# Kernel tuning notes

Measured on AMD Instinct MI355X. Metric: run time of the kernel, lower is better.

## Reference

```python
import jax, jax.numpy as jnp
import numpy as np

N = 131072   # batch of trajectory points
DX = 2       # state dim (module hardcodes Linear(2,300) in vv)
H_TM = 100   # taskmap coupling-layer hidden
H_VV = 300   # vv net hidden
H_VS = 100   # vel-scalar coupling-layer hidden


def setup_inputs() -> dict:
    key = jax.random.key(0)
    ks = iter(jax.random.split(key, 40))
    def W(i, o):
        return jax.random.normal(next(ks), (i, o), jnp.float32) / np.float32(np.sqrt(i))
    def b(o):
        return 0.01 * jax.random.normal(next(ks), (o,), jnp.float32)
    d = {"x": jax.random.normal(next(ks), (N, DX), jnp.float32)}
    # taskmap CouplingLayer nn1 (tanh MLP, residual)
    d.update(tm1_w1=W(DX, H_TM), tm1_b1=b(H_TM), tm1_w2=W(H_TM, H_TM), tm1_b2=b(H_TM), tm1_w3=W(H_TM, DX), tm1_b3=b(DX))
    # taskmap CouplingLayer nn2_1 (elu MLP -> softplus gate)
    d.update(tm2_w1=W(DX, H_TM), tm2_b1=b(H_TM), tm2_w2=W(H_TM, H_TM), tm2_b2=b(H_TM), tm2_w3=W(H_TM, DX), tm2_b3=b(DX))
    # vv net: Linear(2,300) PReLU Linear(300,300) PReLU Linear(300,2)
    d.update(vv_w1=W(DX, H_VV), vv_b1=b(H_VV), vv_a1=jnp.full((1,), 0.25, jnp.float32),
             vv_w2=W(H_VV, H_VV), vv_b2=b(H_VV), vv_a2=jnp.full((1,), 0.25, jnp.float32),
             vv_w3=W(H_VV, DX), vv_b3=b(DX))
    # log_vel_scalar CouplingLayer nn3 (leaky_relu MLP, residual via broadcast)
    d.update(vs_w1=W(DX, H_VS), vs_b1=b(H_VS), vs_w2=W(H_VS, H_VS), vs_b2=b(H_VS), vs_w3=W(H_VS, 1), vs_b3=b(1))
    return d


def reference(x, tm1_w1, tm1_b1, tm1_w2, tm1_b2, tm1_w3, tm1_b3,
              tm2_w1, tm2_b1, tm2_w2, tm2_b2, tm2_w3, tm2_b3,
              vv_w1, vv_b1, vv_a1, vv_w2, vv_b2, vv_a2, vv_w3, vv_b3,
              vs_w1, vs_b1, vs_w2, vs_b2, vs_w3, vs_b3):
    def taskmap(z):  # CouplingLayer forward with is_diffeomorphism=True; z (..., DX)
        h = jnp.tanh(z @ tm1_w1 + tm1_b1)
        h = jnp.tanh(h @ tm1_w2 + tm1_b2)
        y1 = h @ tm1_w3 + tm1_b3 + z
        g = jax.nn.elu(y1 @ tm2_w1 + tm2_b1)
        g = jax.nn.elu(g @ tm2_w2 + tm2_b2)
        s = jax.nn.softplus(g @ tm2_w3 + tm2_b3)
        return s * y1 + y1

    prelu = lambda t, a: jnp.where(t >= 0, t, a * t)
    leaky = lambda t: jnp.where(t >= 0, t, 0.01 * t)

    origin_y = taskmap(jnp.zeros((1, DX), x.dtype))        # taskmap_fcn(origin)
    y = taskmap(x) - origin_y                              # y_hat (N, DX)
    J = jax.vmap(jax.jacfwd(taskmap))(x)                   # J_hat (N, DX, DX)

    # doty_pre = vv(y_hat)
    h = prelu(y @ vv_w1 + vv_b1, vv_a1)
    h = prelu(h @ vv_w2 + vv_b2, vv_a2)
    doty = h @ vv_w3 + vv_b3                               # (N, DX)

    ls_var = jnp.sum(doty * y, axis=-1, keepdims=True)     # (N, 1)
    V_y = jnp.sum(y * y, axis=-1, keepdims=True)           # (N, 1)
    yd = doty - jax.nn.relu(ls_var + 1e-4 * V_y) * y / (V_y + 1e-12)

    J_inv = jnp.linalg.pinv(J)                             # batched pseudo-inverse
    yd_n = yd / jnp.maximum(jnp.linalg.norm(yd, axis=-1, keepdims=True), 1e-12)  # F.normalize
    xd_hat = jnp.einsum('nij,nj->ni', J_inv, yd_n)         # bmm then squeeze

    # vel_scalar = exp(log_vel_scalar(x)) + eps;  log_vel_scalar = nn3(x) + x  (broadcast (N,1)+(N,DX))
    hs = leaky(x @ vs_w1 + vs_b1)
    hs = leaky(hs @ vs_w2 + vs_b2)
    logv = (hs @ vs_w3 + vs_b3) + x                        # (N, DX) via broadcast
    xd = (jnp.exp(logv) + 1e-12) * xd_hat
    return xd
```

## Files before the change

kernel.cpp:

```cpp
#include <hip/hip_runtime.h>
#include <math.h>

#define H1 100
#define H3 300

#define WT_TM1    0
#define WT_TM2    14336
#define WT_VS     28672
#define WT_VV     43008
#define NSHORT    140288
#define F_TM1W1   0
#define F_TM1B1   256
#define F_TM2W1   384
#define F_TM2B1   640
#define F_VSW1    768
#define F_VSB1    1024
#define F_VVW1    1152
#define F_VVB1    1792
#define F_TM1B2   2112
#define F_TM2B2   2240
#define F_VSB2    2368
#define F_VVB2    2496
#define F_TM1W3T  2816
#define F_TM2W3T  3072
#define F_VSW3T   3328
#define F_VVW3T   3456
#define NFLOAT    4096

typedef __attribute__((ext_vector_type(8))) short s8v;
typedef __attribute__((ext_vector_type(4))) float f4v;

__device__ __forceinline__ f4v mfma16(s8v a, s8v b, f4v c) {
    return __builtin_amdgcn_mfma_f32_16x16x32_bf16(a, b, c, 0, 0, 0);
}
__device__ __forceinline__ float rcp_fast(float v) { return __builtin_amdgcn_rcpf(v); }
__device__ __forceinline__ float tanh_fast(float v) {
    float t = __expf(2.f * v);
    return 1.f - 2.f * rcp_fast(t + 1.f);
}
__device__ __forceinline__ float leakyf(float v) { return v >= 0.f ? v : 0.01f * v; }
__device__ __forceinline__ float preluf(float v, float a) { return v >= 0.f ? v : a * v; }
__device__ __forceinline__ short f2bf(float f) {
    union { float f; unsigned u; } v; v.f = f;
    unsigned r = v.u + 0x7fffu + ((v.u >> 16) & 1u);
    return (short)(r >> 16);
}
#define RED4(v) { v += __shfl_xor(v, 16, 64); v += __shfl_xor(v, 32, 64); }

__global__ void ngdv_prep(
    const float* __restrict__ tm1_w1, const float* __restrict__ tm1_b1,
    const float* __restrict__ tm1_w2, const float* __restrict__ tm1_b2,
    const float* __restrict__ tm1_w3, const float* __restrict__ tm1_b3,
    const float* __restrict__ tm2_w1, const float* __restrict__ tm2_b1,
    const float* __restrict__ tm2_w2, const float* __restrict__ tm2_b2,
    const float* __restrict__ tm2_w3, const float* __restrict__ tm2_b3,
    const float* __restrict__ vs_w1,  const float* __restrict__ vs_b1,
    const float* __restrict__ vs_w2,  const float* __restrict__ vs_b2,
    const float* __restrict__ vs_w3,
    const float* __restrict__ vv_w1,  const float* __restrict__ vv_b1,
    const float* __restrict__ vv_w2,  const float* __restrict__ vv_b2,
    const float* __restrict__ vv_w3,
    short* __restrict__ wsb, float* __restrict__ wsf, float* __restrict__ origin_out)
{
    const int tid = threadIdx.x;
    if (blockIdx.x < 564) {
        int idx = blockIdx.x * 256 + tid;
        if (idx < NSHORT) {
            short o;
            if (idx < WT_VV) {
                int rgn = idx / 14336, r = idx % 14336;
                const float* src = (rgn == 0) ? tm1_w2 : (rgn == 1) ? tm2_w2 : vs_w2;
                int nt = r >> 11, ks = (r >> 9) & 3, lane = (r >> 3) & 63, e = r & 7;
                int n = nt*16 + (lane & 15);
                int k = ks*32 + (lane >> 4)*8 + e;
                o = (n < H1 && k < H1) ? f2bf(src[k*H1 + n]) : (short)0;
            } else {
                int r = idx - WT_VV;
                int nt = r / 5120, rem = r % 5120;
                int ks = rem >> 9, lane = (rem >> 3) & 63, e = r & 7;
                int n = nt*16 + (lane & 15);
                int k = ks*32 + (lane >> 4)*8 + e;
                o = (n < H3 && k < H3) ? f2bf(vv_w2[k*H3 + n]) : (short)0;
            }
            wsb[idx] = o;
        } else {
            int f = idx - NSHORT;
            if (f < NFLOAT) {
                float v = 0.f;
                if (f < 256)       { int d = f >> 7, c = f & 127; if (c < H1) v = tm1_w1[d*H1 + c]; }
                else if (f < 384)  { int c = f - 256;  if (c < H1) v = tm1_b1[c]; }
                else if (f < 640)  { int r = f - 384, d = r >> 7, c = r & 127; if (c < H1) v = tm2_w1[d*H1 + c]; }
                else if (f < 768)  { int c = f - 640;  if (c < H1) v = tm2_b1[c]; }
                else if (f < 1024) { int r = f - 768, d = r >> 7, c = r & 127; if (c < H1) v = vs_w1[d*H1 + c]; }
                else if (f < 1152) { int c = f - 1024; if (c < H1) v = vs_b1[c]; }
                else if (f < 1792) { int r = f - 1152, d = r / 320, c = r % 320; if (c < H3) v = vv_w1[d*H3 + c]; }
                else if (f < 2112) { int c = f - 1792; if (c < H3) v = vv_b1[c]; }
                else if (f < 2240) { int c = f - 2112; if (c < H1) v = tm1_b2[c]; }
                else if (f < 2368) { int c = f - 2240; if (c < H1) v = tm2_b2[c]; }
                else if (f < 2496) { int c = f - 2368; if (c < H1) v = vs_b2[c]; }
                else if (f < 2816) { int c = f - 2496; if (c < H3) v = vv_b2[c]; }
                else if (f < 3072) { int r = f - 2816, i = r >> 7, c = r & 127; if (c < H1) v = tm1_w3[c*2 + i]; }
                else if (f < 3328) { int r = f - 3072, i = r >> 7, c = r & 127; if (c < H1) v = tm2_w3[c*2 + i]; }
                else if (f < 3456) { int c = f - 3328; if (c < H1) v = vs_w3[c]; }
                else               { int r = f - 3456, i = r / 320, c = r % 320; if (c < H3) v = vv_w3[c*2 + i]; }
                wsf[f] = v;
            }
        }
        return;
    }
    __shared__ float h1[H1], h2[H1], y1o[2], g1[H1], g2[H1];
    const int r = tid >> 1, hf = tid & 1;
    const int k0 = hf ? 50 : 0, k1 = hf ? 100 : 50;
    if (tid < H1) h1[tid] = tanhf(tm1_b1[tid]);
    __syncthreads();
    {
        float acc = 0.f;
        if (r < H1) for (int k = k0; k < k1; ++k) acc += h1[k] * tm1_w2[k*H1 + r];
        acc += __shfl_xor(acc, 1, 64);
        if (r < H1 && !hf) h2[r] = tanhf(acc + tm1_b2[r]);
    }
    __syncthreads();
    if (tid < 128) {
        int i = tid >> 6, ln = tid & 63;
        float acc = 0.f;
        if (ln < H1) acc += h2[ln] * tm1_w3[ln*2 + i];
        if (ln + 64 < H1) acc += h2[ln+64] * tm1_w3[(ln+64)*2 + i];
        #pragma unroll
        for (int off = 32; off >= 1; off >>= 1) acc += __shfl_xor(acc, off, 64);
        if (ln == 0) y1o[i] = acc + tm1_b3[i];
    }
    __syncthreads();
    if (tid < H1) {
        float pre = tm2_b1[tid] + y1o[0]*tm2_w1[tid] + y1o[1]*tm2_w1[H1 + tid];
        g1[tid] = pre > 0.f ? pre : expm1f(pre);
    }
    __syncthreads();
    {
        float acc = 0.f;
        if (r < H1) for (int k = k0; k < k1; ++k) acc += g1[k] * tm2_w2[k*H1 + r];
        acc += __shfl_xor(acc, 1, 64);
        if (r < H1 && !hf) { float a = acc + tm2_b2[r]; g2[r] = a > 0.f ? a : expm1f(a); }
    }
    __syncthreads();
    if (tid < 128) {
        int i = tid >> 6, ln = tid & 63;
        float acc = 0.f;
        if (ln < H1) acc += g2[ln] * tm2_w3[ln*2 + i];
        if (ln + 64 < H1) acc += g2[ln+64] * tm2_w3[(ln+64)*2 + i];
        #pragma unroll
        for (int off = 32; off >= 1; off >>= 1) acc += __shfl_xor(acc, off, 64);
        if (ln == 0) {
            float a = acc + tm2_b3[i];
            float s = a > 20.f ? a : log1pf(expf(a));
            origin_out[i] = (1.f + s) * y1o[i];
        }
    }
}

__global__ __launch_bounds__(512, 2) void ngdv_main(
    const float* __restrict__ x,
    const float* __restrict__ tm1_b3, const float* __restrict__ tm2_b3,
    const float* __restrict__ vs_b3,  const float* __restrict__ vv_b3,
    const float* __restrict__ vv_a1,  const float* __restrict__ vv_a2,
    const short* __restrict__ wsb,    const float* __restrict__ wsf,
    const float* __restrict__ origin, float* __restrict__ out, int npts)
{
    __shared__ __align__(16) float LW[4096];
    __shared__ __align__(16) short WB[14336];

    const int tid = threadIdx.x;
    const int wv = tid >> 6, lane = tid & 63;
    const int fm = lane & 15, fq = lane >> 4;
    const int p = blockIdx.x*128 + wv*16 + fm;
    float2 xv = {0.f, 0.f};
    if (p < npts) xv = *(const float2*)&x[p*2];
    const float og0 = origin[0], og1 = origin[1];

    for (int i = tid; i < 1024; i += 512) ((f4v*)LW)[i] = ((const f4v*)wsf)[i];
    {
        const s8v* s = (const s8v*)(wsb + WT_TM1);
        s8v* d = (s8v*)WB;
        for (int i = tid; i < 1792; i += 512) d[i] = s[i];
    }
    __syncthreads();
    const float a1v = vv_a1[0], a2v = vv_a2[0];

    s8v afp[4], aft0[4], aft1[4];

    #pragma unroll
    for (int ks = 0; ks < 4; ++ks) {
        int c0 = ks*32 + fq*8;
        #pragma unroll
        for (int hh = 0; hh < 2; ++hh) {
            f4v w0 = *(const f4v*)&LW[F_TM1W1 + c0 + hh*4];
            f4v w1 = *(const f4v*)&LW[F_TM1W1 + 128 + c0 + hh*4];
            f4v bv = *(const f4v*)&LW[F_TM1B1 + c0 + hh*4];
            #pragma unroll
            for (int e = 0; e < 4; ++e) {
                int ee = hh*4 + e;
                float pre = fmaf(xv.y, w1[e], fmaf(xv.x, w0[e], bv[e]));
                float h = tanh_fast(pre), dd = 1.f - h*h;
                afp[ks][ee] = f2bf(h);
                aft0[ks][ee] = f2bf(w0[e]*dd);
                aft1[ks][ee] = f2bf(w1[e]*dd);
            }
        }
    }

    float y1p0 = 0.f, y1p1 = 0.f, dyp00 = 0.f, dyp01 = 0.f, dyp10 = 0.f, dyp11 = 0.f;
    #pragma unroll
    for (int nt = 0; nt < 7; ++nt) {
        s8v b0 = *(const s8v*)&WB[(nt*4+0)*512 + lane*8];
        s8v b1 = *(const s8v*)&WB[(nt*4+1)*512 + lane*8];
        s8v b2 = *(const s8v*)&WB[(nt*4+2)*512 + lane*8];
        s8v b3 = *(const s8v*)&WB[(nt*4+3)*512 + lane*8];
        f4v cp = {0,0,0,0}, ct0 = {0,0,0,0}, ct1 = {0,0,0,0};
        cp  = mfma16(b0, afp[0], cp);   cp  = mfma16(b1, afp[1], cp);
        cp  = mfma16(b2, afp[2], cp);   cp  = mfma16(b3, afp[3], cp);
        ct0 = mfma16(b0, aft0[0], ct0); ct0 = mfma16(b1, aft0[1], ct0);
        ct0 = mfma16(b2, aft0[2], ct0); ct0 = mfma16(b3, aft0[3], ct0);
        ct1 = mfma16(b0, aft1[0], ct1); ct1 = mfma16(b1, aft1[1], ct1);
        ct1 = mfma16(b2, aft1[2], ct1); ct1 = mfma16(b3, aft1[3], ct1);
        int col0 = nt*16 + fq*4;
        f4v bb2 = *(const f4v*)&LW[F_TM1B2 + col0];
        f4v w0v = *(const f4v*)&LW[F_TM1W3T + col0];
        f4v w1v = *(const f4v*)&LW[F_TM1W3T + 128 + col0];
        #pragma unroll
        for (int r = 0; r < 4; ++r) {
            float h = tanh_fast(cp[r] + bb2[r]);
            float dd = 1.f - h*h;
            float t0 = ct0[r]*dd, t1 = ct1[r]*dd;
            y1p0  = fmaf(h,  w0v[r], y1p0);  y1p1  = fmaf(h,  w1v[r], y1p1);
            dyp00 = fmaf(t0, w0v[r], dyp00); dyp01 = fmaf(t0, w1v[r], dyp01);
            dyp10 = fmaf(t1, w0v[r], dyp10); dyp11 = fmaf(t1, w1v[r], dyp11);
        }
    }
    RED4(y1p0); RED4(y1p1); RED4(dyp00); RED4(dyp01); RED4(dyp10); RED4(dyp11);
    const float y10 = y1p0 + tm1_b3[0] + xv.x;
    const float y11 = y1p1 + tm1_b3[1] + xv.y;
    const float dy00 = dyp00 + 1.f, dy01 = dyp01;
    const float dy10 = dyp10, dy11 = dyp11 + 1.f;
    __syncthreads();

    {
        const s8v* s = (const s8v*)(wsb + WT_TM2);
        s8v* d = (s8v*)WB;
        for (int i = tid; i < 1792; i += 512) d[i] = s[i];
    }
    __syncthreads();

    #pragma unroll
    for (int ks = 0; ks < 4; ++ks) {
        int c0 = ks*32 + fq*8;
        #pragma unroll
        for (int hh = 0; hh < 2; ++hh) {
            f4v w0 = *(const f4v*)&LW[F_TM2W1 + c0 + hh*4];
            f4v w1 = *(const f4v*)&LW[F_TM2W1 + 128 + c0 + hh*4];
            f4v bv = *(const f4v*)&LW[F_TM2B1 + c0 + hh*4];
            #pragma unroll
            for (int e = 0; e < 4; ++e) {
                int ee = hh*4 + e;
                float pre = fmaf(y11, w1[e], fmaf(y10, w0[e], bv[e]));
                float g = pre > 0.f ? pre : (__expf(pre) - 1.f);
                float dd = pre > 0.f ? 1.f : (g + 1.f);
                afp[ks][ee] = f2bf(g);
                aft0[ks][ee] = f2bf((dy00*w0[e] + dy01*w1[e]) * dd);
                aft1[ks][ee] = f2bf((dy10*w0[e] + dy11*w1[e]) * dd);
            }
        }
    }

    float spp0 = 0.f, spp1 = 0.f, dsp00 = 0.f, dsp01 = 0.f, dsp10 = 0.f, dsp11 = 0.f;
    #pragma unroll
    for (int nt = 0; nt < 7; ++nt) {
        s8v b0 = *(const s8v*)&WB[(nt*4+0)*512 + lane*8];
        s8v b1 = *(const s8v*)&WB[(nt*4+1)*512 + lane*8];
        s8v b2 = *(const s8v*)&WB[(nt*4+2)*512 + lane*8];
        s8v b3 = *(const s8v*)&WB[(nt*4+3)*512 + lane*8];
        f4v cp = {0,0,0,0}, ct0 = {0,0,0,0}, ct1 = {0,0,0,0};
        cp  = mfma16(b0, afp[0], cp);   cp  = mfma16(b1, afp[1], cp);
        cp  = mfma16(b2, afp[2], cp);   cp  = mfma16(b3, afp[3], cp);
        ct0 = mfma16(b0, aft0[0], ct0); ct0 = mfma16(b1, aft0[1], ct0);
        ct0 = mfma16(b2, aft0[2], ct0); ct0 = mfma16(b3, aft0[3], ct0);
        ct1 = mfma16(b0, aft1[0], ct1); ct1 = mfma16(b1, aft1[1], ct1);
        ct1 = mfma16(b2, aft1[2], ct1); ct1 = mfma16(b3, aft1[3], ct1);
        int col0 = nt*16 + fq*4;
        f4v bb2 = *(const f4v*)&LW[F_TM2B2 + col0];
        f4v w0v = *(const f4v*)&LW[F_TM2W3T + col0];
        f4v w1v = *(const f4v*)&LW[F_TM2W3T + 128 + col0];
        #pragma unroll
        for (int r = 0; r < 4; ++r) {
            float pre = cp[r] + bb2[r];
            float g = pre > 0.f ? pre : (__expf(pre) - 1.f);
            float dd = pre > 0.f ? 1.f : (g + 1.f);
            float t0 = ct0[r]*dd, t1 = ct1[r]*dd;
            spp0  = fmaf(g,  w0v[r], spp0);  spp1  = fmaf(g,  w1v[r], spp1);
            dsp00 = fmaf(t0, w0v[r], dsp00); dsp01 = fmaf(t0, w1v[r], dsp01);
            dsp10 = fmaf(t1, w0v[r], dsp10); dsp11 = fmaf(t1, w1v[r], dsp11);
        }
    }
    RED4(spp0); RED4(spp1); RED4(dsp00); RED4(dsp01); RED4(dsp10); RED4(dsp11);
    float ys0, ys1, Ja, Jb, Jc, Jd;
    {
        float sp0 = spp0 + tm2_b3[0], sp1 = spp1 + tm2_b3[1];
        float s0 = sp0 > 20.f ? sp0 : __logf(1.f + __expf(sp0));
        float s1 = sp1 > 20.f ? sp1 : __logf(1.f + __expf(sp1));
        float sg0 = rcp_fast(1.f + __expf(-sp0));
        float sg1 = rcp_fast(1.f + __expf(-sp1));
        Ja = dsp00*sg0*y10 + (1.f + s0)*dy00;
        Jb = dsp10*sg0*y10 + (1.f + s0)*dy10;
        Jc = dsp01*sg1*y11 + (1.f + s1)*dy01;
        Jd = dsp11*sg1*y11 + (1.f + s1)*dy11;
        ys0 = (1.f + s0)*y10 - og0;
        ys1 = (1.f + s1)*y11 - og1;
    }
    __syncthreads();

    {
        const s8v* s = (const s8v*)(wsb + WT_VS);
        s8v* d = (s8v*)WB;
        for (int i = tid; i < 1792; i += 512) d[i] = s[i];
    }
    __syncthreads();

    #pragma unroll
    for (int ks = 0; ks < 4; ++ks) {
        int c0 = ks*32 + fq*8;
        #pragma unroll
        for (int hh = 0; hh < 2; ++hh) {
            f4v w0 = *(const f4v*)&LW[F_VSW1 + c0 + hh*4];
            f4v w1 = *(const f4v*)&LW[F_VSW1 + 128 + c0 + hh*4];
            f4v bv = *(const f4v*)&LW[F_VSB1 + c0 + hh*4];
            #pragma unroll
            for (int e = 0; e < 4; ++e)
                afp[ks][hh*4+e] = f2bf(leakyf(fmaf(xv.y, w1[e], fmaf(xv.x, w0[e], bv[e]))));
        }
    }

    float lvp = 0.f;
    #pragma unroll
    for (int nt = 0; nt < 7; ++nt) {
        s8v b0 = *(const s8v*)&WB[(nt*4+0)*512 + lane*8];
        s8v b1 = *(const s8v*)&WB[(nt*4+1)*512 + lane*8];
        s8v b2 = *(const s8v*)&WB[(nt*4+2)*512 + lane*8];
        s8v b3 = *(const s8v*)&WB[(nt*4+3)*512 + lane*8];
        f4v cp = {0,0,0,0};
        cp = mfma16(b0, afp[0], cp); cp = mfma16(b1, afp[1], cp);
        cp = mfma16(b2, afp[2], cp); cp = mfma16(b3, afp[3], cp);
        int col0 = nt*16 + fq*4;
        f4v bb2 = *(const f4v*)&LW[F_VSB2 + col0];
        f4v w0v = *(const f4v*)&LW[F_VSW3T + col0];
        #pragma unroll
        for (int r = 0; r < 4; ++r)
            lvp = fmaf(leakyf(cp[r] + bb2[r]), w0v[r], lvp);
    }
    RED4(lvp);
    const float lv = lvp + vs_b3[0];
    __syncthreads();

    {
        const s8v* s = (const s8v*)(wsb + WT_VV);
        s8v* d = (s8v*)WB;
        for (int i = tid; i < 640; i += 512) d[i] = s[i];
    }
    s8v afw[10];
    #pragma unroll
    for (int ks = 0; ks < 10; ++ks) {
        int c0 = ks*32 + fq*8;
        #pragma unroll
        for (int hh = 0; hh < 2; ++hh) {
            f4v w0 = *(const f4v*)&LW[F_VVW1 + c0 + hh*4];
            f4v w1 = *(const f4v*)&LW[F_VVW1 + 320 + c0 + hh*4];
            f4v bv = *(const f4v*)&LW[F_VVB1 + c0 + hh*4];
            #pragma unroll
            for (int e = 0; e < 4; ++e)
                afw[ks][hh*4+e] = f2bf(preluf(fmaf(ys1, w1[e], fmaf(ys0, w0[e], bv[e])), a1v));
        }
    }
    __syncthreads();

    float dtp0 = 0.f, dtp1 = 0.f;
    for (int t = 0; t < 19; ++t) {
        if (t < 18) {
            const s8v* s = (const s8v*)(wsb + WT_VV + (t+1)*5120);
            s8v* d = (s8v*)(WB + ((t+1) & 1)*5120);
            for (int i = tid; i < 640; i += 512) d[i] = s[i];
        }
        const short* VB = WB + (t & 1)*5120;
        f4v cp = {0,0,0,0};
        #pragma unroll
        for (int ks = 0; ks < 10; ++ks) {
            s8v bf = *(const s8v*)&VB[ks*512 + lane*8];
            cp = mfma16(bf, afw[ks], cp);
        }
        int col0 = t*16 + fq*4;
        f4v bb2 = *(const f4v*)&LW[F_VVB2 + col0];
        f4v w0v = *(const f4v*)&LW[F_VVW3T + col0];
        f4v w1v = *(const f4v*)&LW[F_VVW3T + 320 + col0];
        #pragma unroll
        for (int r = 0; r < 4; ++r) {
            float v = preluf(cp[r] + bb2[r], a2v);
            dtp0 = fmaf(v, w0v[r], dtp0);
            dtp1 = fmaf(v, w1v[r], dtp1);
        }
        __syncthreads();
    }
    RED4(dtp0); RED4(dtp1);
    const float dt0 = dtp0 + vv_b3[0];
    const float dt1 = dtp1 + vv_b3[1];

    if (fq == 0 && p < npts) {
        float ls = dt0*ys0 + dt1*ys1;
        float Vq = ys0*ys0 + ys1*ys1;
        float coef = fmaxf(ls + 1e-4f*Vq, 0.f) * rcp_fast(Vq + 1e-12f);
        float yd0 = dt0 - coef*ys0, yd1 = dt1 - coef*ys1;
        float inv_n = rcp_fast(fmaxf(sqrtf(yd0*yd0 + yd1*yd1), 1e-12f));
        float yn0 = yd0*inv_n, yn1 = yd1*inv_n;
        float invdet = rcp_fast(Ja*Jd - Jb*Jc);
        float xh0 = ( Jd*yn0 - Jb*yn1) * invdet;
        float xh1 = (-Jc*yn0 + Ja*yn1) * invdet;
        float2 o;
        o.x = (__expf(lv + xv.x) + 1e-12f) * xh0;
        o.y = (__expf(lv + xv.y) + 1e-12f) * xh1;
        *(float2*)&out[p*2] = o;
    }
}

extern "C" void kernel_launch(void* const* d_in, const int* in_sizes, int n_in,
                              void* d_out, int out_size, void* d_ws, size_t ws_size,
                              hipStream_t stream) {
    const float* x      = (const float*)d_in[0];
    const float* tm1_w1 = (const float*)d_in[1];
    const float* tm1_b1 = (const float*)d_in[2];
    const float* tm1_w2 = (const float*)d_in[3];
    const float* tm1_b2 = (const float*)d_in[4];
    const float* tm1_w3 = (const float*)d_in[5];
    const float* tm1_b3 = (const float*)d_in[6];
    const float* tm2_w1 = (const float*)d_in[7];
    const float* tm2_b1 = (const float*)d_in[8];
    const float* tm2_w2 = (const float*)d_in[9];
    const float* tm2_b2 = (const float*)d_in[10];
    const float* tm2_w3 = (const float*)d_in[11];
    const float* tm2_b3 = (const float*)d_in[12];
    const float* vv_w1  = (const float*)d_in[13];
    const float* vv_b1  = (const float*)d_in[14];
    const float* vv_a1  = (const float*)d_in[15];
    const float* vv_w2  = (const float*)d_in[16];
    const float* vv_b2  = (const float*)d_in[17];
    const float* vv_a2  = (const float*)d_in[18];
    const float* vv_w3  = (const float*)d_in[19];
    const float* vv_b3  = (const float*)d_in[20];
    const float* vs_w1  = (const float*)d_in[21];
    const float* vs_b1  = (const float*)d_in[22];
    const float* vs_w2  = (const float*)d_in[23];
    const float* vs_b2  = (const float*)d_in[24];
    const float* vs_w3  = (const float*)d_in[25];
    const float* vs_b3  = (const float*)d_in[26];

    float* out       = (float*)d_out;
    float* origin_ws = (float*)d_ws;
    short* wsb       = (short*)((char*)d_ws + 64);
    float* wsf       = (float*)((char*)d_ws + 64 + NSHORT*2);
    const int npts = in_sizes[0] / 2;
    const int nblk = (npts + 127) / 128;

    ngdv_prep<<<565, 256, 0, stream>>>(
        tm1_w1, tm1_b1, tm1_w2, tm1_b2, tm1_w3, tm1_b3,
        tm2_w1, tm2_b1, tm2_w2, tm2_b2, tm2_w3, tm2_b3,
        vs_w1, vs_b1, vs_w2, vs_b2, vs_w3,
        vv_w1, vv_b1, vv_w2, vv_b2, vv_w3,
        wsb, wsf, origin_ws);

    ngdv_main<<<nblk, 512, 0, stream>>>(
        x, tm1_b3, tm2_b3, vs_b3, vv_b3, vv_a1, vv_a2,
        wsb, wsf, origin_ws, out, npts);
}
```

Measured before the change: 255.5 us.

## Halve block size to 256 threads and read first-layer weights from global memory

Shrinks the main kernel's block from 512 to 256 threads (64 points per block, launch bounds 256,4), doubling the grid. It also stops staging the first-layer weights and biases in shared memory and reads them straight from the global workspace, which halves the float shared buffer. The aim is to raise occupancy and cut per-block shared memory and barrier cost. In exchange each block now copies the full bf16 weight tiles for half as many points, and the first-layer loads go through the cache hierarchy instead of LDS.

```diff
diff --git a/kernel.cpp b/kernel.cpp
--- a/kernel.cpp
+++ b/kernel.cpp
@@ -26,6 +26,8 @@
 #define F_VSW3T   3328
 #define F_VVW3T   3456
 #define NFLOAT    4096
+#define LWB       2112
+#define LWN       1984
 
 typedef __attribute__((ext_vector_type(8))) short s8v;
 typedef __attribute__((ext_vector_type(4))) float f4v;
@@ -157,7 +159,7 @@
     }
 }
 
-__global__ __launch_bounds__(512, 2) void ngdv_main(
+__global__ __launch_bounds__(256, 4) void ngdv_main(
     const float* __restrict__ x,
     const float* __restrict__ tm1_b3, const float* __restrict__ tm2_b3,
     const float* __restrict__ vs_b3,  const float* __restrict__ vv_b3,
@@ -165,22 +167,22 @@
     const short* __restrict__ wsb,    const float* __restrict__ wsf,
     const float* __restrict__ origin, float* __restrict__ out, int npts)
 {
-    __shared__ __align__(16) float LW[4096];
+    __shared__ __align__(16) float LW[2048];
     __shared__ __align__(16) short WB[14336];
 
     const int tid = threadIdx.x;
     const int wv = tid >> 6, lane = tid & 63;
     const int fm = lane & 15, fq = lane >> 4;
-    const int p = blockIdx.x*128 + wv*16 + fm;
+    const int p = blockIdx.x*64 + wv*16 + fm;
     float2 xv = {0.f, 0.f};
     if (p < npts) xv = *(const float2*)&x[p*2];
     const float og0 = origin[0], og1 = origin[1];
 
-    for (int i = tid; i < 1024; i += 512) ((f4v*)LW)[i] = ((const f4v*)wsf)[i];
+    for (int i = tid; i < 496; i += 256) ((f4v*)LW)[i] = *(const f4v*)&wsf[LWB + i*4];
     {
         const s8v* s = (const s8v*)(wsb + WT_TM1);
         s8v* d = (s8v*)WB;
-        for (int i = tid; i < 1792; i += 512) d[i] = s[i];
+        for (int i = tid; i < 1792; i += 256) d[i] = s[i];
     }
     __syncthreads();
     const float a1v = vv_a1[0], a2v = vv_a2[0];
@@ -192,9 +194,9 @@
         int c0 = ks*32 + fq*8;
         #pragma unroll
         for (int hh = 0; hh < 2; ++hh) {
-            f4v w0 = *(const f4v*)&LW[F_TM1W1 + c0 + hh*4];
-            f4v w1 = *(const f4v*)&LW[F_TM1W1 + 128 + c0 + hh*4];
-            f4v bv = *(const f4v*)&LW[F_TM1B1 + c0 + hh*4];
+            f4v w0 = *(const f4v*)&wsf[F_TM1W1 + c0 + hh*4];
+            f4v w1 = *(const f4v*)&wsf[F_TM1W1 + 128 + c0 + hh*4];
+            f4v bv = *(const f4v*)&wsf[F_TM1B1 + c0 + hh*4];
             #pragma unroll
             for (int e = 0; e < 4; ++e) {
                 int ee = hh*4 + e;
@@ -222,9 +224,9 @@
         ct1 = mfma16(b0, aft1[0], ct1); ct1 = mfma16(b1, aft1[1], ct1);
         ct1 = mfma16(b2, aft1[2], ct1); ct1 = mfma16(b3, aft1[3], ct1);
         int col0 = nt*16 + fq*4;
-        f4v bb2 = *(const f4v*)&LW[F_TM1B2 + col0];
-        f4v w0v = *(const f4v*)&LW[F_TM1W3T + col0];
-        f4v w1v = *(const f4v*)&LW[F_TM1W3T + 128 + col0];
+        f4v bb2 = *(const f4v*)&LW[F_TM1B2 - LWB + col0];
+        f4v w0v = *(const f4v*)&LW[F_TM1W3T - LWB + col0];
+        f4v w1v = *(const f4v*)&LW[F_TM1W3T + 128 - LWB + col0];
         #pragma unroll
         for (int r = 0; r < 4; ++r) {
             float h = tanh_fast(cp[r] + bb2[r]);
@@ -245,7 +247,7 @@
     {
         const s8v* s = (const s8v*)(wsb + WT_TM2);
         s8v* d = (s8v*)WB;
-        for (int i = tid; i < 1792; i += 512) d[i] = s[i];
+        for (int i = tid; i < 1792; i += 256) d[i] = s[i];
     }
     __syncthreads();
 
@@ -254,9 +256,9 @@
         int c0 = ks*32 + fq*8;
         #pragma unroll
         for (int hh = 0; hh < 2; ++hh) {
-            f4v w0 = *(const f4v*)&LW[F_TM2W1 + c0 + hh*4];
-            f4v w1 = *(const f4v*)&LW[F_TM2W1 + 128 + c0 + hh*4];
-            f4v bv = *(const f4v*)&LW[F_TM2B1 + c0 + hh*4];
+            f4v w0 = *(const f4v*)&wsf[F_TM2W1 + c0 + hh*4];
+            f4v w1 = *(const f4v*)&wsf[F_TM2W1 + 128 + c0 + hh*4];
+            f4v bv = *(const f4v*)&wsf[F_TM2B1 + c0 + hh*4];
             #pragma unroll
             for (int e = 0; e < 4; ++e) {
                 int ee = hh*4 + e;
@@ -285,9 +287,9 @@
         ct1 = mfma16(b0, aft1[0], ct1); ct1 = mfma16(b1, aft1[1], ct1);
         ct1 = mfma16(b2, aft1[2], ct1); ct1 = mfma16(b3, aft1[3], ct1);
         int col0 = nt*16 + fq*4;
-        f4v bb2 = *(const f4v*)&LW[F_TM2B2 + col0];
-        f4v w0v = *(const f4v*)&LW[F_TM2W3T + col0];
-        f4v w1v = *(const f4v*)&LW[F_TM2W3T + 128 + col0];
+        f4v bb2 = *(const f4v*)&LW[F_TM2B2 - LWB + col0];
+        f4v w0v = *(const f4v*)&LW[F_TM2W3T - LWB + col0];
+        f4v w1v = *(const f4v*)&LW[F_TM2W3T + 128 - LWB + col0];
         #pragma unroll
         for (int r = 0; r < 4; ++r) {
             float pre = cp[r] + bb2[r];
@@ -319,7 +321,7 @@
     {
         const s8v* s = (const s8v*)(wsb + WT_VS);
         s8v* d = (s8v*)WB;
-        for (int i = tid; i < 1792; i += 512) d[i] = s[i];
+        for (int i = tid; i < 1792; i += 256) d[i] = s[i];
     }
     __syncthreads();
 
@@ -328,9 +330,9 @@
         int c0 = ks*32 + fq*8;
         #pragma unroll
         for (int hh = 0; hh < 2; ++hh) {
-            f4v w0 = *(const f4v*)&LW[F_VSW1 + c0 + hh*4];
-            f4v w1 = *(const f4v*)&LW[F_VSW1 + 128 + c0 + hh*4];
-            f4v bv = *(const f4v*)&LW[F_VSB1 + c0 + hh*4];
+            f4v w0 = *(const f4v*)&wsf[F_VSW1 + c0 + hh*4];
+            f4v w1 = *(const f4v*)&wsf[F_VSW1 + 128 + c0 + hh*4];
+            f4v bv = *(const f4v*)&wsf[F_VSB1 + c0 + hh*4];
             #pragma unroll
             for (int e = 0; e < 4; ++e)
                 afp[ks][hh*4+e] = f2bf(leakyf(fmaf(xv.y, w1[e], fmaf(xv.x, w0[e], bv[e]))));
@@ -348,8 +350,8 @@
         cp = mfma16(b0, afp[0], cp); cp = mfma16(b1, afp[1], cp);
         cp = mfma16(b2, afp[2], cp); cp = mfma16(b3, afp[3], cp);
         int col0 = nt*16 + fq*4;
-        f4v bb2 = *(const f4v*)&LW[F_VSB2 + col0];
-        f4v w0v = *(const f4v*)&LW[F_VSW3T + col0];
+        f4v bb2 = *(const f4v*)&LW[F_VSB2 - LWB + col0];
+        f4v w0v = *(const f4v*)&LW[F_VSW3T - LWB + col0];
         #pragma unroll
         for (int r = 0; r < 4; ++r)
             lvp = fmaf(leakyf(cp[r] + bb2[r]), w0v[r], lvp);
@@ -361,7 +363,7 @@
     {
         const s8v* s = (const s8v*)(wsb + WT_VV);
         s8v* d = (s8v*)WB;
-        for (int i = tid; i < 640; i += 512) d[i] = s[i];
+        for (int i = tid; i < 640; i += 256) d[i] = s[i];
     }
     s8v afw[10];
     #pragma unroll
@@ -369,9 +371,9 @@
         int c0 = ks*32 + fq*8;
         #pragma unroll
         for (int hh = 0; hh < 2; ++hh) {
-            f4v w0 = *(const f4v*)&LW[F_VVW1 + c0 + hh*4];
-            f4v w1 = *(const f4v*)&LW[F_VVW1 + 320 + c0 + hh*4];
-            f4v bv = *(const f4v*)&LW[F_VVB1 + c0 + hh*4];
+            f4v w0 = *(const f4v*)&wsf[F_VVW1 + c0 + hh*4];
+            f4v w1 = *(const f4v*)&wsf[F_VVW1 + 320 + c0 + hh*4];
+            f4v bv = *(const f4v*)&wsf[F_VVB1 + c0 + hh*4];
             #pragma unroll
             for (int e = 0; e < 4; ++e)
                 afw[ks][hh*4+e] = f2bf(preluf(fmaf(ys1, w1[e], fmaf(ys0, w0[e], bv[e])), a1v));
@@ -384,7 +386,7 @@
         if (t < 18) {
             const s8v* s = (const s8v*)(wsb + WT_VV + (t+1)*5120);
             s8v* d = (s8v*)(WB + ((t+1) & 1)*5120);
-            for (int i = tid; i < 640; i += 512) d[i] = s[i];
+            for (int i = tid; i < 640; i += 256) d[i] = s[i];
         }
         const short* VB = WB + (t & 1)*5120;
         f4v cp = {0,0,0,0};
@@ -394,9 +396,9 @@
             cp = mfma16(bf, afw[ks], cp);
         }
         int col0 = t*16 + fq*4;
-        f4v bb2 = *(const f4v*)&LW[F_VVB2 + col0];
-        f4v w0v = *(const f4v*)&LW[F_VVW3T + col0];
-        f4v w1v = *(const f4v*)&LW[F_VVW3T + 320 + col0];
+        f4v bb2 = *(const f4v*)&LW[F_VVB2 - LWB + col0];
+        f4v w0v = *(const f4v*)&LW[F_VVW3T - LWB + col0];
+        f4v w1v = *(const f4v*)&LW[F_VVW3T + 320 - LWB + col0];
         #pragma unroll
         for (int r = 0; r < 4; ++r) {
             float v = preluf(cp[r] + bb2[r], a2v);
@@ -462,7 +464,7 @@
     short* wsb       = (short*)((char*)d_ws + 64);
     float* wsf       = (float*)((char*)d_ws + 64 + NSHORT*2);
     const int npts = in_sizes[0] / 2;
-    const int nblk = (npts + 127) / 128;
+    const int nblk = (npts + 63) / 64;
 
     ngdv_prep<<<565, 256, 0, stream>>>(
         tm1_w1, tm1_b1, tm1_w2, tm1_b2, tm1_w3, tm1_b3,
@@ -471,7 +473,7 @@
         vv_w1, vv_b1, vv_w2, vv_b2, vv_w3,
         wsb, wsf, origin_ws);
 
-    ngdv_main<<<nblk, 512, 0, stream>>>(
+    ngdv_main<<<nblk, 256, 0, stream>>>(
         x, tm1_b3, tm2_b3, vs_b3, vv_b3, vv_a1, vv_a2,
         wsb, wsf, origin_ws, out, npts);
 }
```

Measured after the change: 244.2 us. 4.4% less time.
